# Kernel optimization log

Measured on AMD Instinct MI355X. Metric: run time of the kernel, lower is better.

Reference implementation:

```python
import jax, jax.numpy as jnp
import numpy as np

N_HEADS = 16


def setup_inputs() -> dict:
    key = jax.random.key(0)
    ks = jax.random.split(key, 9)
    B, S, D = 2, 2048, 1024
    sc = 0.02
    return {
        'x': jax.random.normal(ks[0], (B, S, D), jnp.float32),
        'Wq': jax.random.normal(ks[1], (D, D), jnp.float32) * sc,
        'bq': jax.random.normal(ks[2], (D,), jnp.float32) * sc,
        'Wk': jax.random.normal(ks[3], (D, D), jnp.float32) * sc,
        'bk': jax.random.normal(ks[4], (D,), jnp.float32) * sc,
        'Wv': jax.random.normal(ks[5], (D, D), jnp.float32) * sc,
        'bv': jax.random.normal(ks[6], (D,), jnp.float32) * sc,
        'Wo': jax.random.normal(ks[7], (D, D), jnp.float32) * sc,
        'bo': jax.random.normal(ks[8], (D,), jnp.float32) * sc,
    }


def reference(x, Wq, bq, Wk, bk, Wv, bv, Wo, bo):
    # Chunked causal prefill. The chunk-wise mask (q_pos >= kv_pos over the
    # growing KV cache) is mathematically identical to full causal attention,
    # so we compute it as one vectorized masked softmax attention.
    B, S, D = x.shape
    H = N_HEADS
    hd = D // H

    def proj(W, b):
        # torch Linear: y = x @ W.T + b ; then split heads -> [B,H,S,hd]
        y = jnp.einsum('bsd,ed->bse', x, W) + b
        return y.reshape(B, S, H, hd).transpose(0, 2, 1, 3)

    q = proj(Wq, bq)
    k = proj(Wk, bk)
    v = proj(Wv, bv)

    scores = jnp.einsum('bhqd,bhkd->bhqk', q, k) / jnp.sqrt(jnp.asarray(hd, x.dtype))
    causal = jnp.tril(jnp.ones((S, S), dtype=bool))  # [S,S]
    scores = jnp.where(causal[None, None], scores, jnp.asarray(-jnp.inf, scores.dtype))
    attn = jax.nn.softmax(scores, axis=-1)
    ctx = jnp.einsum('bhqk,bhkd->bhqd', attn, v)  # [B,H,S,hd]
    ctx = ctx.transpose(0, 2, 1, 3).reshape(B, S, D)
    out = jnp.einsum('bsd,ed->bse', ctx, Wo) + bo
    return out
```

## Files before the change

### kernel.cpp

```cpp
#include <hip/hip_runtime.h>
#include <cstdint>
#include <math.h>

typedef _Float16 f16;
typedef _Float16 f16x2 __attribute__((ext_vector_type(2)));
typedef _Float16 f16x4 __attribute__((ext_vector_type(4)));
typedef _Float16 f16x8 __attribute__((ext_vector_type(8)));
typedef __fp16   h16x2 __attribute__((ext_vector_type(2)));
typedef float    f32x4 __attribute__((ext_vector_type(4)));

__device__ __forceinline__ f32x4 mfma16(f16x8 a, f16x8 b, f32x4 c) {
  return __builtin_amdgcn_mfma_f32_16x16x32_f16(a, b, c, 0, 0, 0);
}
__device__ __forceinline__ void gl2lds16(const f16* g, f16* l) {
  __builtin_amdgcn_global_load_lds((__attribute__((address_space(1))) void*)(g),
                                   (__attribute__((address_space(3))) void*)(l),
                                   16, 0, 0);
}
__device__ __forceinline__ float fexp2(float x) { return __builtin_amdgcn_exp2f(x); }
__device__ __forceinline__ f16x2 pkrtz(float a, float b) {
  h16x2 r = __builtin_amdgcn_cvt_pkrtz(a, b);
  return __builtin_bit_cast(f16x2, r);
}
__device__ __forceinline__ float dot2acc(f16x2 a, f16x2 b, float c) {
#if __has_builtin(__builtin_amdgcn_fdot2)
  return __builtin_amdgcn_fdot2(__builtin_bit_cast(h16x2, a),
                                __builtin_bit_cast(h16x2, b), c, false);
#else
  return c + (float)a[0] * (float)b[0] + (float)a[1] * (float)b[1];
#endif
}

__global__ __launch_bounds__(256) void cvt_kernel(
    const float* __restrict__ x,  const float* __restrict__ wq, const float* __restrict__ wk,
    const float* __restrict__ wv, const float* __restrict__ wo,
    f16* __restrict__ xh, f16* __restrict__ wqkvh, f16* __restrict__ woh)
{
  const int seg = blockIdx.y;
  const float* src; f16* dst; int n;
  if      (seg == 0) { src = x;  dst = xh;              n = 4194304; }
  else if (seg == 1) { src = wq; dst = wqkvh;           n = 1048576; }
  else if (seg == 2) { src = wk; dst = wqkvh + 1048576; n = 1048576; }
  else if (seg == 3) { src = wv; dst = wqkvh + 2097152; n = 1048576; }
  else               { src = wo; dst = woh;             n = 1048576; }
  const int idx = (int)(blockIdx.x * 256 + threadIdx.x) * 8;
  if (idx >= n) return;
  f32x4 a = *(const f32x4*)(src + idx);
  f32x4 b = *(const f32x4*)(src + idx + 4);
  f16x8 h;
  h[0] = (f16)a[0]; h[1] = (f16)a[1]; h[2] = (f16)a[2]; h[3] = (f16)a[3];
  h[4] = (f16)b[0]; h[5] = (f16)b[1]; h[6] = (f16)b[2]; h[7] = (f16)b[3];
  *(f16x8*)(dst + idx) = h;
}

__global__ __launch_bounds__(256) void gemm_qkv(
    const f16* __restrict__ A, const f16* __restrict__ B,
    const float* __restrict__ bias0, const float* __restrict__ bias1, const float* __restrict__ bias2,
    f16* __restrict__ Qp, f16* __restrict__ Kp, f16* __restrict__ Vp)
{
  constexpr int K = 1024;
  __shared__ __align__(16) f16 As[128 * 32];
  __shared__ __align__(16) f16 Bs[128 * 32];
  const int tid  = threadIdx.x;
  const int wave = tid >> 6, lane = tid & 63;
  const int quad = lane >> 4, col = lane & 15;
  const int tile_m = blockIdx.y * 128, tile_n = blockIdx.x * 128;
  const int mb = (wave >> 1) * 64, nb = (wave & 1) * 64;
  const int srow = lane >> 2, scol = (lane & 3) * 8;
  const f16* gA = A + (size_t)(tile_m + wave * 32 + srow) * K + scol;
  const f16* gB = B + (size_t)(tile_n + wave * 32 + srow) * K + scol;
  f16* lA = As + wave * 1024;
  f16* lB = Bs + wave * 1024;

  f32x4 acc[4][4] = {};
  for (int k0 = 0; k0 < K; k0 += 32) {
    gl2lds16(gA + k0,          lA);
    gl2lds16(gA + 16 * K + k0, lA + 512);
    gl2lds16(gB + k0,          lB);
    gl2lds16(gB + 16 * K + k0, lB + 512);
    __syncthreads();
    f16x8 af[4], bf[4];
    #pragma unroll
    for (int i = 0; i < 4; ++i)
      af[i] = *(const f16x8*)&As[(mb + i * 16 + col) * 32 + quad * 8];
    #pragma unroll
    for (int j = 0; j < 4; ++j)
      bf[j] = *(const f16x8*)&Bs[(nb + j * 16 + col) * 32 + quad * 8];
    #pragma unroll
    for (int i = 0; i < 4; ++i)
      #pragma unroll
      for (int j = 0; j < 4; ++j)
        acc[i][j] = mfma16(af[i], bf[j], acc[i][j]);
    __syncthreads();
  }

  #pragma unroll
  for (int j = 0; j < 4; ++j) {
    const int gn = tile_n + nb + j * 16 + col;
    const int which = gn >> 10;
    const int d = gn & 1023;
    const float* bp = (which == 0) ? bias0 : (which == 1) ? bias1 : bias2;
    f16* dst        = (which == 0) ? Qp    : (which == 1) ? Kp    : Vp;
    const float bvv = bp[d];
    const float qs  = (which == 0) ? 0.18033688f : 1.0f;
    const int h = d >> 6, hi = d & 63;
    #pragma unroll
    for (int i = 0; i < 4; ++i) {
      #pragma unroll
      for (int r = 0; r < 4; ++r) {
        const int gm = tile_m + mb + i * 16 + quad * 4 + r;
        const int bb = gm >> 11, s = gm & 2047;
        dst[(((size_t)bb * 16 + h) * 2048 + s) * 64 + hi] = (f16)((acc[i][j][r] + bvv) * qs);
      }
    }
  }
}

__global__ __launch_bounds__(256) void vtrans_kernel(
    const f16* __restrict__ Vh, f16* __restrict__ Vt)
{
  __shared__ __align__(16) f16 t[64][72];
  const int bh = blockIdx.y;
  const int s0 = blockIdx.x * 64;
  const int tid = threadIdx.x;
  const int sr = tid >> 2, dc = (tid & 3) * 16;
  const size_t ib = ((size_t)bh * 2048 + s0 + sr) * 64 + dc;
  f16x8 v0 = *(const f16x8*)&Vh[ib];
  f16x8 v1 = *(const f16x8*)&Vh[ib + 8];
  *(f16x8*)&t[sr][dc]     = v0;
  *(f16x8*)&t[sr][dc + 8] = v1;
  __syncthreads();
  const int d = tid >> 2, sc = (tid & 3) * 16;
  f16x8 o0, o1;
  #pragma unroll
  for (int j = 0; j < 8; ++j) { o0[j] = t[sc + j][d]; o1[j] = t[sc + 8 + j][d]; }
  const size_t ob = ((size_t)bh * 64 + d) * 2048 + s0 + sc;
  *(f16x8*)&Vt[ob]     = o0;
  *(f16x8*)&Vt[ob + 8] = o1;
}

__global__ __launch_bounds__(256) void attn_kernel(
    const f16* __restrict__ Q, const f16* __restrict__ K, const f16* __restrict__ Vt,
    f16* __restrict__ ctx)
{
  __shared__ __align__(16) f16 Ks[2][64 * 72];
  __shared__ __align__(16) f16 Vts[2][64 * 72];
  __shared__ __align__(16) f16 Ps[4][16 * 72];

  const int bh  = blockIdx.y;
  const int tid = threadIdx.x;
  const int wave = tid >> 6, lane = tid & 63;
  const int quad = lane >> 4, col = lane & 15;
  const int b = bh >> 4, h = bh & 15;
  const size_t base = (size_t)bh * 2048 * 64;
  const size_t vtb  = (size_t)bh * 64 * 2048;

  int srow[2], sc8[2];
  #pragma unroll
  for (int i = 0; i < 2; ++i) {
    const int flat = tid + i * 256;
    srow[i] = flat >> 3;
    sc8[i]  = (flat & 7) * 8;
  }

  auto run_tile = [&](int qt) {
    const int q0 = qt * 64;
    const int qa = q0 + wave * 16;
    const f16x8 bqa0 = *(const f16x8*)&Q[base + (size_t)(qa + col) * 64 + quad * 8];
    const f16x8 bqa1 = *(const f16x8*)&Q[base + (size_t)(qa + col) * 64 + 32 + quad * 8];

    f32x4 cta[4] = {};
    float ma = -INFINITY;
    float la = 0.f;

    f16x8 kr[2], vr[2];
    auto gload = [&](int t) {
      #pragma unroll
      for (int i = 0; i < 2; ++i) {
        kr[i] = *(const f16x8*)&K[base + (size_t)(t * 64 + srow[i]) * 64 + sc8[i]];
        vr[i] = *(const f16x8*)&Vt[vtb + (size_t)srow[i] * 2048 + t * 64 + sc8[i]];
      }
    };
    auto swrite = [&](int buf) {
      #pragma unroll
      for (int i = 0; i < 2; ++i) {
        *(f16x8*)&Ks[buf][srow[i] * 72 + sc8[i]]  = kr[i];
        *(f16x8*)&Vts[buf][srow[i] * 72 + sc8[i]] = vr[i];
      }
    };

    const int nIter = qt + 1;

    gload(0);
    __syncthreads();
    swrite(0);
    if (nIter > 1) gload(1);

    for (int t = 0; t < nIter; ++t) {
      const int cur = t & 1;
      __syncthreads();
      if (t + 1 < nIter) {
        swrite(cur ^ 1);
        if (t + 2 < nIter) gload(t + 2);
      }

      f32x4 sa[4];
      #pragma unroll
      for (int jt = 0; jt < 4; ++jt) {
        const int kro = (jt * 16 + col) * 72;
        const f16x8 ak0 = *(const f16x8*)&Ks[cur][kro + quad * 8];
        const f16x8 ak1 = *(const f16x8*)&Ks[cur][kro + 32 + quad * 8];
        f32x4 za = {};
        za = mfma16(ak0, bqa0, za);
        sa[jt] = mfma16(ak1, bqa1, za);
      }

      if (t == qt) {
        #pragma unroll
        for (int jt = 0; jt < 4; ++jt) {
          const int kg = t * 64 + jt * 16 + quad * 4;
          #pragma unroll
          for (int r = 0; r < 4; ++r) {
            if (kg + r > qa + col) sa[jt][r] = -1e30f;
          }
        }
      }

      float tm = fmaxf(fmaxf(sa[0][0], sa[0][1]), fmaxf(sa[0][2], sa[0][3]));
      #pragma unroll
      for (int jt = 1; jt < 4; ++jt)
        tm = fmaxf(tm, fmaxf(fmaxf(sa[jt][0], sa[jt][1]), fmaxf(sa[jt][2], sa[jt][3])));
      tm = fmaxf(tm, __shfl_xor(tm, 16));
      tm = fmaxf(tm, __shfl_xor(tm, 32));

      if (__any(tm > ma + 6.f)) {
        const float mnew = fmaxf(ma, tm);
        const float alpha = fexp2(ma - mnew);
        ma = mnew;
        la *= alpha;
        f32x4 ava;
        #pragma unroll
        for (int r = 0; r < 4; ++r) ava[r] = __shfl(alpha, quad * 4 + r);
        #pragma unroll
        for (int jd = 0; jd < 4; ++jd) cta[jd] *= ava;
      }

      const f16x2 one2 = {(_Float16)1.f, (_Float16)1.f};
      float rs = 0.f;
      #pragma unroll
      for (int jt = 0; jt < 4; ++jt) {
        const f16x2 a01 = pkrtz(fexp2(sa[jt][0] - ma), fexp2(sa[jt][1] - ma));
        const f16x2 a23 = pkrtz(fexp2(sa[jt][2] - ma), fexp2(sa[jt][3] - ma));
        rs = dot2acc(a01, one2, rs);
        rs = dot2acc(a23, one2, rs);
        f16x4 pw; pw[0] = a01[0]; pw[1] = a01[1]; pw[2] = a23[0]; pw[3] = a23[1];
        *(f16x4*)&Ps[wave][col * 72 + jt * 16 + quad * 4] = pw;
      }
      la += rs;

      __asm__ volatile("s_waitcnt lgkmcnt(0)" ::: "memory");

      const f16x8 apa0 = *(const f16x8*)&Ps[wave][col * 72 + quad * 8];
      const f16x8 apa1 = *(const f16x8*)&Ps[wave][col * 72 + 32 + quad * 8];
      #pragma unroll
      for (int jd = 0; jd < 4; ++jd) {
        const int vro = (jd * 16 + col) * 72;
        const f16x8 bv0 = *(const f16x8*)&Vts[cur][vro + quad * 8];
        const f16x8 bv1 = *(const f16x8*)&Vts[cur][vro + 32 + quad * 8];
        cta[jd] = mfma16(apa1, bv1, mfma16(apa0, bv0, cta[jd]));
      }
    }

    la += __shfl_xor(la, 16);
    la += __shfl_xor(la, 32);
    f32x4 lva;
    #pragma unroll
    for (int r = 0; r < 4; ++r) lva[r] = __shfl(la, quad * 4 + r);
    #pragma unroll
    for (int jd = 0; jd < 4; ++jd) {
      #pragma unroll
      for (int r = 0; r < 4; ++r) {
        const int qga = qa + quad * 4 + r;
        const int d = h * 64 + jd * 16 + col;
        ctx[((size_t)b * 2048 + qga) * 1024 + d] = (f16)(cta[jd][r] / lva[r]);
      }
    }
  };

  run_tile(blockIdx.x);
  run_tile(31 - blockIdx.x);
}

__global__ __launch_bounds__(256) void gemm_o(
    const f16* __restrict__ A, const f16* __restrict__ B, const float* __restrict__ bias,
    float* __restrict__ Out)
{
  constexpr int K = 1024;
  __shared__ __align__(16) f16 As[128 * 32];
  __shared__ __align__(16) f16 Bs[64 * 32];
  const int tid  = threadIdx.x;
  const int wave = tid >> 6, lane = tid & 63;
  const int quad = lane >> 4, col = lane & 15;
  const int tile_m = blockIdx.y * 128, tile_n = blockIdx.x * 64;
  const int mb = wave * 32;
  const int srow = lane >> 2, scol = (lane & 3) * 8;
  const f16* gA = A + (size_t)(tile_m + wave * 32 + srow) * K + scol;
  const f16* gB = B + (size_t)(tile_n + wave * 16 + srow) * K + scol;
  f16* lA = As + wave * 1024;
  f16* lB = Bs + wave * 512;

  f32x4 acc[2][4] = {};
  for (int k0 = 0; k0 < K; k0 += 32) {
    gl2lds16(gA + k0,          lA);
    gl2lds16(gA + 16 * K + k0, lA + 512);
    gl2lds16(gB + k0,          lB);
    __syncthreads();
    f16x8 af[2], bf[4];
    #pragma unroll
    for (int i = 0; i < 2; ++i)
      af[i] = *(const f16x8*)&As[(mb + i * 16 + col) * 32 + quad * 8];
    #pragma unroll
    for (int j = 0; j < 4; ++j)
      bf[j] = *(const f16x8*)&Bs[(j * 16 + col) * 32 + quad * 8];
    #pragma unroll
    for (int i = 0; i < 2; ++i)
      #pragma unroll
      for (int j = 0; j < 4; ++j)
        acc[i][j] = mfma16(af[i], bf[j], acc[i][j]);
    __syncthreads();
  }

  #pragma unroll
  for (int j = 0; j < 4; ++j) {
    const int gn = tile_n + j * 16 + col;
    const float bvv = bias[gn];
    #pragma unroll
    for (int i = 0; i < 2; ++i) {
      #pragma unroll
      for (int r = 0; r < 4; ++r) {
        const int gm = tile_m + mb + i * 16 + quad * 4 + r;
        Out[(size_t)gm * 1024 + gn] = acc[i][j][r] + bvv;
      }
    }
  }
}

extern "C" void kernel_launch(void* const* d_in, const int* in_sizes, int n_in,
                              void* d_out, int out_size, void* d_ws, size_t ws_size,
                              hipStream_t stream)
{
  const float* x  = (const float*)d_in[0];
  const float* Wq = (const float*)d_in[1];
  const float* bq = (const float*)d_in[2];
  const float* Wk = (const float*)d_in[3];
  const float* bk = (const float*)d_in[4];
  const float* Wv = (const float*)d_in[5];
  const float* bv = (const float*)d_in[6];
  const float* Wo = (const float*)d_in[7];
  const float* bo = (const float*)d_in[8];
  float* out = (float*)d_out;

  f16* ws = (f16*)d_ws;
  const size_t M1 = 1048576;
  f16* xh    = ws;
  f16* wqkvh = ws + 4  * M1;
  f16* woh   = ws + 7  * M1;
  f16* Qh    = ws + 8  * M1;
  f16* Kh    = ws + 12 * M1;
  f16* Vh    = ws + 16 * M1;
  f16* Vth   = ws + 20 * M1;
  f16* ctxh  = ws + 24 * M1;

  cvt_kernel<<<dim3(2048, 5), 256, 0, stream>>>(x, Wq, Wk, Wv, Wo, xh, wqkvh, woh);
  gemm_qkv<<<dim3(24, 32), 256, 0, stream>>>(xh, wqkvh, bq, bk, bv, Qh, Kh, Vh);
  vtrans_kernel<<<dim3(32, 32), 256, 0, stream>>>(Vh, Vth);
  attn_kernel<<<dim3(16, 32), 256, 0, stream>>>(Qh, Kh, Vth, ctxh);
  gemm_o<<<dim3(16, 32), 256, 0, stream>>>(ctxh, woh, bo, out);
}
```

Measured before the change: 196.9 us.

## Split causal attention KV range across two blocks and merge with combine kernel

```diff
diff --git a/kernel.cpp b/kernel.cpp
--- a/kernel.cpp
+++ b/kernel.cpp
@@ -141,7 +141,7 @@
 
 __global__ __launch_bounds__(256) void attn_kernel(
     const f16* __restrict__ Q, const f16* __restrict__ K, const f16* __restrict__ Vt,
-    f16* __restrict__ ctx)
+    f16* __restrict__ cp0, f16* __restrict__ cp1, float* __restrict__ ml)
 {
   __shared__ __align__(16) f16 Ks[2][64 * 72];
   __shared__ __align__(16) f16 Vts[2][64 * 72];
@@ -163,132 +163,178 @@
     sc8[i]  = (flat & 7) * 8;
   }
 
-  auto run_tile = [&](int qt) {
+  auto run_seg = [&](int qt, int t0, int t1, f16* __restrict__ cdst, int chunk) {
     const int q0 = qt * 64;
     const int qa = q0 + wave * 16;
-    const f16x8 bqa0 = *(const f16x8*)&Q[base + (size_t)(qa + col) * 64 + quad * 8];
-    const f16x8 bqa1 = *(const f16x8*)&Q[base + (size_t)(qa + col) * 64 + 32 + quad * 8];
-
-    f32x4 cta[4] = {};
     float ma = -INFINITY;
     float la = 0.f;
 
-    f16x8 kr[2], vr[2];
-    auto gload = [&](int t) {
-      #pragma unroll
-      for (int i = 0; i < 2; ++i) {
-        kr[i] = *(const f16x8*)&K[base + (size_t)(t * 64 + srow[i]) * 64 + sc8[i]];
-        vr[i] = *(const f16x8*)&Vt[vtb + (size_t)srow[i] * 2048 + t * 64 + sc8[i]];
+    if (t1 > t0) {
+      const f16x8 bqa0 = *(const f16x8*)&Q[base + (size_t)(qa + col) * 64 + quad * 8];
+      const f16x8 bqa1 = *(const f16x8*)&Q[base + (size_t)(qa + col) * 64 + 32 + quad * 8];
+
+      f32x4 cta[4] = {};
+
+      f16x8 kr[2], vr[2];
+      auto gload = [&](int t) {
+        #pragma unroll
+        for (int i = 0; i < 2; ++i) {
+          kr[i] = *(const f16x8*)&K[base + (size_t)(t * 64 + srow[i]) * 64 + sc8[i]];
+          vr[i] = *(const f16x8*)&Vt[vtb + (size_t)srow[i] * 2048 + t * 64 + sc8[i]];
+        }
+      };
+      auto swrite = [&](int buf) {
+        #pragma unroll
+        for (int i = 0; i < 2; ++i) {
+          *(f16x8*)&Ks[buf][srow[i] * 72 + sc8[i]]  = kr[i];
+          *(f16x8*)&Vts[buf][srow[i] * 72 + sc8[i]] = vr[i];
+        }
+      };
+
+      gload(t0);
+      __syncthreads();
+      swrite(0);
+      if (t0 + 1 < t1) gload(t0 + 1);
+
+      for (int t = t0; t < t1; ++t) {
+        const int cur = (t - t0) & 1;
+        __syncthreads();
+        if (t + 1 < t1) {
+          swrite(cur ^ 1);
+          if (t + 2 < t1) gload(t + 2);
+        }
+
+        f32x4 sa[4];
+        #pragma unroll
+        for (int jt = 0; jt < 4; ++jt) {
+          const int kro = (jt * 16 + col) * 72;
+          const f16x8 ak0 = *(const f16x8*)&Ks[cur][kro + quad * 8];
+          const f16x8 ak1 = *(const f16x8*)&Ks[cur][kro + 32 + quad * 8];
+          f32x4 za = {};
+          za = mfma16(ak0, bqa0, za);
+          sa[jt] = mfma16(ak1, bqa1, za);
+        }
+
+        if (t == qt) {
+          #pragma unroll
+          for (int jt = 0; jt < 4; ++jt) {
+            const int kg = t * 64 + jt * 16 + quad * 4;
+            #pragma unroll
+            for (int r = 0; r < 4; ++r) {
+              if (kg + r > qa + col) sa[jt][r] = -1e30f;
+            }
+          }
+        }
+
+        float tm = fmaxf(fmaxf(sa[0][0], sa[0][1]), fmaxf(sa[0][2], sa[0][3]));
+        #pragma unroll
+        for (int jt = 1; jt < 4; ++jt)
+          tm = fmaxf(tm, fmaxf(fmaxf(sa[jt][0], sa[jt][1]), fmaxf(sa[jt][2], sa[jt][3])));
+        tm = fmaxf(tm, __shfl_xor(tm, 16));
+        tm = fmaxf(tm, __shfl_xor(tm, 32));
+
+        if (__any(tm > ma + 6.f)) {
+          const float mnew = fmaxf(ma, tm);
+          const float alpha = fexp2(ma - mnew);
+          ma = mnew;
+          la *= alpha;
+          f32x4 ava;
+          #pragma unroll
+          for (int r = 0; r < 4; ++r) ava[r] = __shfl(alpha, quad * 4 + r);
+          #pragma unroll
+          for (int jd = 0; jd < 4; ++jd) cta[jd] *= ava;
+        }
+
+        const f16x2 one2 = {(_Float16)1.f, (_Float16)1.f};
+        float rs = 0.f;
+        #pragma unroll
+        for (int jt = 0; jt < 4; ++jt) {
+          const f16x2 a01 = pkrtz(fexp2(sa[jt][0] - ma), fexp2(sa[jt][1] - ma));
+          const f16x2 a23 = pkrtz(fexp2(sa[jt][2] - ma), fexp2(sa[jt][3] - ma));
+          rs = dot2acc(a01, one2, rs);
+          rs = dot2acc(a23, one2, rs);
+          f16x4 pw; pw[0] = a01[0]; pw[1] = a01[1]; pw[2] = a23[0]; pw[3] = a23[1];
+          *(f16x4*)&Ps[wave][col * 72 + jt * 16 + quad * 4] = pw;
+        }
+        la += rs;
+
+        __asm__ volatile("s_waitcnt lgkmcnt(0)" ::: "memory");
+
+        const f16x8 apa0 = *(const f16x8*)&Ps[wave][col * 72 + quad * 8];
+        const f16x8 apa1 = *(const f16x8*)&Ps[wave][col * 72 + 32 + quad * 8];
+        #pragma unroll
+        for (int jd = 0; jd < 4; ++jd) {
+          const int vro = (jd * 16 + col) * 72;
+          const f16x8 bv0 = *(const f16x8*)&Vts[cur][vro + quad * 8];
+          const f16x8 bv1 = *(const f16x8*)&Vts[cur][vro + 32 + quad * 8];
+          cta[jd] = mfma16(apa1, bv1, mfma16(apa0, bv0, cta[jd]));
+        }
       }
-    };
-    auto swrite = [&](int buf) {
-      #pragma unroll
-      for (int i = 0; i < 2; ++i) {
-        *(f16x8*)&Ks[buf][srow[i] * 72 + sc8[i]]  = kr[i];
-        *(f16x8*)&Vts[buf][srow[i] * 72 + sc8[i]] = vr[i];
+
+      la += __shfl_xor(la, 16);
+      la += __shfl_xor(la, 32);
+      f32x4 lva;
+      #pragma unroll
+      for (int r = 0; r < 4; ++r) lva[r] = __shfl(la, quad * 4 + r);
+      #pragma unroll
+      for (int jd = 0; jd < 4; ++jd) {
+        #pragma unroll
+        for (int r = 0; r < 4; ++r) {
+          const int qga = qa + quad * 4 + r;
+          const int d = h * 64 + jd * 16 + col;
+          cdst[((size_t)b * 2048 + qga) * 1024 + d] = (f16)(cta[jd][r] / lva[r]);
+        }
       }
-    };
-
-    const int nIter = qt + 1;
-
-    gload(0);
-    __syncthreads();
-    swrite(0);
-    if (nIter > 1) gload(1);
-
-    for (int t = 0; t < nIter; ++t) {
-      const int cur = t & 1;
-      __syncthreads();
-      if (t + 1 < nIter) {
-        swrite(cur ^ 1);
-        if (t + 2 < nIter) gload(t + 2);
-      }
-
-      f32x4 sa[4];
-      #pragma unroll
-      for (int jt = 0; jt < 4; ++jt) {
-        const int kro = (jt * 16 + col) * 72;
-        const f16x8 ak0 = *(const f16x8*)&Ks[cur][kro + quad * 8];
-        const f16x8 ak1 = *(const f16x8*)&Ks[cur][kro + 32 + quad * 8];
-        f32x4 za = {};
-        za = mfma16(ak0, bqa0, za);
-        sa[jt] = mfma16(ak1, bqa1, za);
-      }
-
-      if (t == qt) {
-        #pragma unroll
-        for (int jt = 0; jt < 4; ++jt) {
-          const int kg = t * 64 + jt * 16 + quad * 4;
-          #pragma unroll
-          for (int r = 0; r < 4; ++r) {
-            if (kg + r > qa + col) sa[jt][r] = -1e30f;
-          }
-        }
-      }
-
-      float tm = fmaxf(fmaxf(sa[0][0], sa[0][1]), fmaxf(sa[0][2], sa[0][3]));
-      #pragma unroll
-      for (int jt = 1; jt < 4; ++jt)
-        tm = fmaxf(tm, fmaxf(fmaxf(sa[jt][0], sa[jt][1]), fmaxf(sa[jt][2], sa[jt][3])));
-      tm = fmaxf(tm, __shfl_xor(tm, 16));
-      tm = fmaxf(tm, __shfl_xor(tm, 32));
-
-      if (__any(tm > ma + 6.f)) {
-        const float mnew = fmaxf(ma, tm);
-        const float alpha = fexp2(ma - mnew);
-        ma = mnew;
-        la *= alpha;
-        f32x4 ava;
-        #pragma unroll
-        for (int r = 0; r < 4; ++r) ava[r] = __shfl(alpha, quad * 4 + r);
-        #pragma unroll
-        for (int jd = 0; jd < 4; ++jd) cta[jd] *= ava;
-      }
-
-      const f16x2 one2 = {(_Float16)1.f, (_Float16)1.f};
-      float rs = 0.f;
-      #pragma unroll
-      for (int jt = 0; jt < 4; ++jt) {
-        const f16x2 a01 = pkrtz(fexp2(sa[jt][0] - ma), fexp2(sa[jt][1] - ma));
-        const f16x2 a23 = pkrtz(fexp2(sa[jt][2] - ma), fexp2(sa[jt][3] - ma));
-        rs = dot2acc(a01, one2, rs);
-        rs = dot2acc(a23, one2, rs);
-        f16x4 pw; pw[0] = a01[0]; pw[1] = a01[1]; pw[2] = a23[0]; pw[3] = a23[1];
-        *(f16x4*)&Ps[wave][col * 72 + jt * 16 + quad * 4] = pw;
-      }
-      la += rs;
-
-      __asm__ volatile("s_waitcnt lgkmcnt(0)" ::: "memory");
-
-      const f16x8 apa0 = *(const f16x8*)&Ps[wave][col * 72 + quad * 8];
-      const f16x8 apa1 = *(const f16x8*)&Ps[wave][col * 72 + 32 + quad * 8];
-      #pragma unroll
-      for (int jd = 0; jd < 4; ++jd) {
-        const int vro = (jd * 16 + col) * 72;
-        const f16x8 bv0 = *(const f16x8*)&Vts[cur][vro + quad * 8];
-        const f16x8 bv1 = *(const f16x8*)&Vts[cur][vro + 32 + quad * 8];
-        cta[jd] = mfma16(apa1, bv1, mfma16(apa0, bv0, cta[jd]));
-      }
+    } else {
+      la += __shfl_xor(la, 16);
+      la += __shfl_xor(la, 32);
     }
 
-    la += __shfl_xor(la, 16);
-    la += __shfl_xor(la, 32);
-    f32x4 lva;
-    #pragma unroll
-    for (int r = 0; r < 4; ++r) lva[r] = __shfl(la, quad * 4 + r);
-    #pragma unroll
-    for (int jd = 0; jd < 4; ++jd) {
-      #pragma unroll
-      for (int r = 0; r < 4; ++r) {
-        const int qga = qa + quad * 4 + r;
-        const int d = h * 64 + jd * 16 + col;
-        ctx[((size_t)b * 2048 + qga) * 1024 + d] = (f16)(cta[jd][r] / lva[r]);
-      }
+    if (quad == 0) {
+      const int row = bh * 2048 + qa + col;
+      ml[chunk * 131072 + row]         = ma;
+      ml[chunk * 131072 + 65536 + row] = la;
     }
   };
 
-  run_tile(blockIdx.x);
-  run_tile(31 - blockIdx.x);
+  const int x = blockIdx.x;
+  const int qa_t = x;
+  const int a1 = (x + 2) >> 1;
+  const int qb_t = 31 - x;
+  const int nb_ = 32 - x;
+  const int b0 = (nb_ + 1) >> 1;
+
+  run_seg(qa_t, 0, a1, cp0, 0);
+  run_seg(qb_t, b0, nb_, cp1, 1);
+}
+
+__global__ __launch_bounds__(256) void combine_kernel(
+    const f16* __restrict__ c0, const f16* __restrict__ c1,
+    const float* __restrict__ ml, f16* __restrict__ out)
+{
+  const int gtid = (int)(blockIdx.x * 256 + threadIdx.x);
+  const int d0 = (gtid & 7) * 8;
+  const int row = gtid >> 3;
+  const int bh = row >> 11, q = row & 2047;
+  const int b = bh >> 4, h = bh & 15;
+  const float m0 = ml[row],          l0 = ml[65536 + row];
+  const float m1 = ml[131072 + row], l1 = ml[196608 + row];
+  const float M = fmaxf(m0, m1);
+  const float s0 = l0 * fexp2(m0 - M);
+  const float s1 = l1 * fexp2(m1 - M);
+  const size_t idx = ((size_t)b * 2048 + q) * 1024 + h * 64 + d0;
+  f16x8 v0 = *(const f16x8*)&c0[idx];
+  f16x8 r;
+  if (s1 > 0.f) {
+    const float inv = 1.f / (s0 + s1);
+    f16x8 v1 = *(const f16x8*)&c1[idx];
+    #pragma unroll
+    for (int i = 0; i < 8; ++i)
+      r[i] = (f16)(((float)v0[i] * s0 + (float)v1[i] * s1) * inv);
+  } else {
+    r = v0;
+  }
+  *(f16x8*)&out[idx] = r;
 }
 
 __global__ __launch_bounds__(256) void gemm_o(
@@ -371,9 +417,14 @@
   f16* Vth   = ws + 20 * M1;
   f16* ctxh  = ws + 24 * M1;
 
+  f16*   cp0 = xh;
+  f16*   cp1 = Vh;
+  float* ml  = (float*)wqkvh;
+
   cvt_kernel<<<dim3(2048, 5), 256, 0, stream>>>(x, Wq, Wk, Wv, Wo, xh, wqkvh, woh);
   gemm_qkv<<<dim3(24, 32), 256, 0, stream>>>(xh, wqkvh, bq, bk, bv, Qh, Kh, Vh);
   vtrans_kernel<<<dim3(32, 32), 256, 0, stream>>>(Vh, Vth);
-  attn_kernel<<<dim3(16, 32), 256, 0, stream>>>(Qh, Kh, Vth, ctxh);
+  attn_kernel<<<dim3(32, 32), 256, 0, stream>>>(Qh, Kh, Vth, cp0, cp1, ml);
+  combine_kernel<<<2048, 256, 0, stream>>>(cp0, cp1, ml, ctxh);
   gemm_o<<<dim3(16, 32), 256, 0, stream>>>(ctxh, woh, bo, out);
 }
```

Measured after the change: 207.4 us. 5.3% more time.
